# Optimization experiments

Hardware: AMD Instinct MI355X
Metric: run time of the kernel (lower is better)

## Reference

```python
import jax, jax.numpy as jnp
import numpy as np

DIM = 1024
NUM_HEADS = 16
HEAD_DIM = DIM // NUM_HEADS


def setup_inputs() -> dict:
    key = jax.random.key(0)
    k1, k2, k3 = jax.random.split(key, 3)
    x = jax.random.normal(k1, (2, 2048, DIM), dtype=jnp.float32)
    # nn.Linear weights stored as [out, in]; apply as x @ W.T
    w_qkv = jax.random.normal(k2, (3 * DIM, DIM), dtype=jnp.float32) * (1.0 / np.sqrt(DIM))
    w_out = jax.random.normal(k3, (DIM, DIM), dtype=jnp.float32) * (1.0 / np.sqrt(DIM))
    return {"x": x, "w_qkv": w_qkv, "w_out": w_out}


def reference(x, w_qkv, w_out):
    b, t, _ = x.shape
    qkv = x @ w_qkv.T                                  # [b, t, 3*dim]
    qkv = qkv.reshape(b, t, 3, NUM_HEADS, HEAD_DIM)    # (three h d) split order
    q, k, v = jnp.moveaxis(qkv, 2, 0)                  # each [b, t, h, d]
    q = q.transpose(0, 2, 1, 3)                        # [b, h, t, d]
    k = k.transpose(0, 2, 1, 3)
    v = v.transpose(0, 2, 1, 3)
    attn = jnp.einsum('bhid,bhjd->bhij', q, k) / np.sqrt(HEAD_DIM)
    causal_mask = jnp.triu(jnp.ones((t, t), dtype=bool), k=1)
    attn = jnp.where(causal_mask, -jnp.inf, attn)
    attn = jax.nn.softmax(attn, axis=-1)
    out = jnp.einsum('bhij,bhjd->bhid', attn, v)
    out = out.transpose(0, 2, 1, 3).reshape(b, t, DIM)
    return out @ w_out.T
```

## Files before the change

### kernel.cpp

```cpp
#include <hip/hip_runtime.h>

#define DIM_ 1024
#define HEADS_ 16
#define HD_ 64
#define T_ 2048
#define BATCH_ 2
#define QKVN_ 3072

typedef unsigned short u16;
typedef unsigned int u32;
typedef float f32x4 __attribute__((ext_vector_type(4)));
typedef float f32x16 __attribute__((ext_vector_type(16)));
typedef short s16x8 __attribute__((ext_vector_type(8)));
typedef unsigned short u16x4 __attribute__((ext_vector_type(4)));

__device__ __forceinline__ u16 f2bf(float f) {
  unsigned u = __float_as_uint(f);
  u += 0x7fffu + ((u >> 16) & 1u);
  return (u16)(u >> 16);
}

__device__ __forceinline__ float fexp2(float x) {
  float r;
  asm("v_exp_f32 %0, %1" : "=v"(r) : "v"(x));
  return r;
}

__device__ __forceinline__ float fmax3(float a, float b, float c) {
  float r;
  asm("v_max3_f32 %0, %1, %2, %3" : "=v"(r) : "v"(a), "v"(b), "v"(c));
  return r;
}

__device__ __forceinline__ u32 cvtpk(float a, float b) {
  u32 r;
  asm("v_cvt_pk_bf16_f32 %0, %1, %2" : "=v"(r) : "v"(a), "v"(b));
  return r;
}

__global__ __launch_bounds__(256) void cvt_all(const float* __restrict__ x,
                                               const float* __restrict__ wqkv,
                                               const float* __restrict__ wout,
                                               u16* __restrict__ outbase) {
  int i = blockIdx.x * 256 + threadIdx.x;
  const float4* src;
  int off;
  if (i < 1048576) { src = (const float4*)x; off = i; }
  else if (i < 1835008) { src = (const float4*)wqkv; off = i - 1048576; }
  else { src = (const float4*)wout; off = i - 1835008; }
  float4 v = src[off];
  u16x4 o;
  o.x = f2bf(v.x); o.y = f2bf(v.y); o.z = f2bf(v.z); o.w = f2bf(v.w);
  reinterpret_cast<u16x4*>(outbase)[i] = o;
}

__device__ __forceinline__ void gld_lds16(const void* g, void* l) {
  auto gp = (__attribute__((address_space(1))) char*)(unsigned long long)g;
  auto lp = (__attribute__((address_space(3))) char*)(unsigned int)(unsigned long long)l;
  __builtin_amdgcn_global_load_lds(gp, lp, 16, 0, 0);
}

template <int MODE>
__global__ __launch_bounds__(256) void gemm1(const u16* __restrict__ A,
                                             const u16* __restrict__ B,
                                             void* __restrict__ Cv,
                                             u16* __restrict__ vto) {
  constexpr int K = 1024;
  constexpr int NN = (MODE == 1) ? 1024 : QKVN_;
  constexpr int NT = (MODE == 1) ? 8 : 24;
  constexpr int CPX = (MODE == 1) ? 32 : 96;
  __shared__ __align__(16) u16 smem[16384];
  u16* As = smem;
  u16* Bs = smem + 8192;
  const int bid = blockIdx.x;
  const int wk = (bid & 7) * CPX + (bid >> 3);
  const int mt = wk / NT, nt = wk % NT;
  const int tid = threadIdx.x;
  const int lane = tid & 63;
  const int w = tid >> 6;
  const int wr = w >> 1, wc = w & 1;
  const int lrow = lane & 15, kg = lane >> 4;
  const u16* Ag = A + (size_t)(mt * 128) * K;
  const u16* Bg = B + (size_t)(nt * 128) * K;

  f32x4 acc[4][4];
#pragma unroll
  for (int i = 0; i < 4; ++i)
#pragma unroll
    for (int j = 0; j < 4; ++j) {
      f32x4 z = {0.f, 0.f, 0.f, 0.f};
      acc[i][j] = z;
    }

  const int srow = tid >> 3;
  const int scol = 8 * ((tid & 7) ^ ((tid >> 3) & 7));
  const int ldsw = (tid & ~63) * 16;

  int aoff[4][2], boff[4][2];
#pragma unroll
  for (int mf = 0; mf < 4; ++mf)
#pragma unroll
    for (int ks = 0; ks < 2; ++ks) {
      aoff[mf][ks] = (wr * 64 + mf * 16 + lrow) * 128 + (((ks * 4 + kg) ^ (lrow & 7)) << 4);
      boff[mf][ks] = (wc * 64 + mf * 16 + lrow) * 128 + (((ks * 4 + kg) ^ (lrow & 7)) << 4);
    }

  for (int k0 = 0; k0 < K; k0 += 64) {
#pragma unroll
    for (int c = 0; c < 4; ++c) {
      gld_lds16(Ag + (size_t)(c * 32 + srow) * K + k0 + scol, (char*)As + c * 4096 + ldsw);
      gld_lds16(Bg + (size_t)(c * 32 + srow) * K + k0 + scol, (char*)Bs + c * 4096 + ldsw);
    }
    __syncthreads();
#pragma unroll
    for (int ks = 0; ks < 2; ++ks) {
      s16x8 a[4], b[4];
#pragma unroll
      for (int mf = 0; mf < 4; ++mf)
        a[mf] = *(const s16x8*)((const char*)As + aoff[mf][ks]);
#pragma unroll
      for (int nf = 0; nf < 4; ++nf)
        b[nf] = *(const s16x8*)((const char*)Bs + boff[nf][ks]);
#pragma unroll
      for (int mf = 0; mf < 4; ++mf)
#pragma unroll
        for (int nf = 0; nf < 4; ++nf)
          acc[mf][nf] = __builtin_amdgcn_mfma_f32_16x16x32_bf16(a[mf], b[nf], acc[mf][nf], 0, 0, 0);
    }
    __syncthreads();
  }

  if (MODE == 1) {
    float* C = (float*)Cv;
#pragma unroll
    for (int mf = 0; mf < 4; ++mf)
#pragma unroll
      for (int nf = 0; nf < 4; ++nf)
#pragma unroll
        for (int j = 0; j < 4; ++j) {
          int r = mt * 128 + wr * 64 + mf * 16 + 4 * kg + j;
          int c = nt * 128 + wc * 64 + nf * 16 + lrow;
          C[(size_t)r * NN + c] = acc[mf][nf][j];
        }
  } else if (nt < 16) {
    u16* qkvo = (u16*)Cv;
#pragma unroll
    for (int mf = 0; mf < 4; ++mf)
#pragma unroll
      for (int nf = 0; nf < 4; ++nf)
#pragma unroll
        for (int j = 0; j < 4; ++j) {
          int r = mt * 128 + wr * 64 + mf * 16 + 4 * kg + j;
          int c = nt * 128 + wc * 64 + nf * 16 + lrow;
          qkvo[(size_t)r * QKVN_ + c] = f2bf(acc[mf][nf][j]);
        }
  } else {
    const int c16 = tid >> 4, chunk = tid & 15;
    const int bb = mt >> 4;
    const int tb = (mt & 15) * 128 + chunk * 8;
#pragma unroll
    for (int p = 0; p < 2; ++p) {
      __syncthreads();
      if (wc == p) {
#pragma unroll
        for (int mf = 0; mf < 4; ++mf)
#pragma unroll
          for (int nf = 0; nf < 4; ++nf) {
            const int cl = nf * 16 + lrow;
            const int rl = wr * 64 + mf * 16 + 4 * kg;
            u16x4 pk;
            pk.x = f2bf(acc[mf][nf][0]); pk.y = f2bf(acc[mf][nf][1]);
            pk.z = f2bf(acc[mf][nf][2]); pk.w = f2bf(acc[mf][nf][3]);
            *(u16x4*)&smem[cl * 136 + rl] = pk;
          }
      }
      __syncthreads();
#pragma unroll
      for (int pp = 0; pp < 4; ++pp) {
        const int cl = pp * 16 + c16;
        const int cg = nt * 128 + p * 64 + cl;
        const int hV = (cg >> 6) & 15, d = cg & 63;
        const s16x8 v = *(const s16x8*)&smem[cl * 136 + chunk * 8];
        *(s16x8*)(vto + ((size_t)((bb * 16 + hV) * 64 + d)) * T_ + tb) = v;
      }
    }
  }
}

__global__ __launch_bounds__(256, 2) void attn_fwd(const u16* __restrict__ qkv,
                                                   const u16* __restrict__ vt,
                                                   u16* __restrict__ o) {
  const int gid = blockIdx.x;
  const int gq = gid >> 3;
  const int bh = (gid & 7) * 4 + (gq >> 4);
  const int pr = gq & 15;
  const int b = bh >> 4, h = bh & 15;
  const int tid = threadIdx.x;
  const int lane = tid & 63;
  const int qw = (tid >> 6) & 1;
  const int kvg = tid >> 7;
  const int l31 = lane & 31, hi = lane >> 5;

  __shared__ __align__(16) char smem[65536];

  const int row_s = tid >> 3, slot_s = tid & 7;
  const u16* Kbase = qkv + (size_t)(b * T_) * QKVN_ + 1024 + h * 64;
  const u16* Vbase = vt + (size_t)(bh * 64) * T_;
  const u16* KgA = Kbase + (size_t)row_s * QKVN_ + slot_s * 8;
  const u16* KgB = KgA + (size_t)32 * QKVN_;
  const u16* VgA = Vbase + (size_t)row_s * T_ + slot_s * 8;
  const u16* VgB = VgA + (size_t)32 * T_;
  const int dstA = row_s * 128 + ((slot_s ^ (row_s & 7)) << 4);

  const int rbyte = l31 * 128;
  const int xsw = l31 & 7;
  const float CEXP = 0.18033688011112042f;

  for (int ph = 0; ph < 2; ++ph) {
    const int jt = (ph == 0) ? (31 - pr) : pr;
    const int nt = jt + 1;
    const int nrt = (nt + 1) >> 1;
    const int qrow0 = 64 * jt + 32 * qw;

    s16x8 qf[4];
    {
      const u16* qp = qkv + (size_t)(b * T_ + qrow0 + l31) * QKVN_ + h * 64 + 8 * hi;
#pragma unroll
      for (int ksl = 0; ksl < 4; ++ksl)
        qf[ksl] = *(const s16x8*)(qp + 16 * ksl);
    }

    f32x16 o0v, o1v;
#pragma unroll
    for (int r = 0; r < 16; ++r) { o0v[r] = 0.f; o1v[r] = 0.f; }
    float mrun = -__builtin_inff(), lrun = 0.0f;

    __syncthreads();
    *(s16x8*)(smem + dstA)                 = *(const s16x8*)KgA;
    *(s16x8*)(smem + 4096 + dstA)          = *(const s16x8*)KgB;
    *(s16x8*)(smem + 32768 + dstA)         = *(const s16x8*)VgA;
    *(s16x8*)(smem + 32768 + 4096 + dstA)  = *(const s16x8*)VgB;
    if (nt > 1) {
      *(s16x8*)(smem + 8192 + dstA)                = *(const s16x8*)(KgA + (size_t)64 * QKVN_);
      *(s16x8*)(smem + 8192 + 4096 + dstA)         = *(const s16x8*)(KgB + (size_t)64 * QKVN_);
      *(s16x8*)(smem + 32768 + 8192 + dstA)        = *(const s16x8*)(VgA + 64);
      *(s16x8*)(smem + 32768 + 8192 + 4096 + dstA) = *(const s16x8*)(VgB + 64);
    }

    int cur = 0;
    for (int r = 0; r < nrt; ++r) {
      const int t = 2 * r + kvg;
      const bool pe = (2 * r + 2 < nt), po = (2 * r + 3 < nt);
      s16x8 ke0, ke1, ve0, ve1, ko0, ko1, vo0, vo1;
      if (pe) {
        const size_t kofs = (size_t)(2 * r + 2) * 64 * QKVN_;
        const int vofs = (2 * r + 2) * 64;
        ke0 = *(const s16x8*)(KgA + kofs);
        ke1 = *(const s16x8*)(KgB + kofs);
        ve0 = *(const s16x8*)(VgA + vofs);
        ve1 = *(const s16x8*)(VgB + vofs);
      }
      if (po) {
        const size_t kofs = (size_t)(2 * r + 3) * 64 * QKVN_;
        const int vofs = (2 * r + 3) * 64;
        ko0 = *(const s16x8*)(KgA + kofs);
        ko1 = *(const s16x8*)(KgB + kofs);
        vo0 = *(const s16x8*)(VgA + vofs);
        vo1 = *(const s16x8*)(VgB + vofs);
      }
      __syncthreads();

      if (t < nt) {
        const char* Kc = smem + cur * 16384 + kvg * 8192;
        const char* Vc = smem + 32768 + cur * 16384 + kvg * 8192;
        const bool isdiag = (t == nt - 1);
        const bool two = !(isdiag && qw == 0);

        f32x16 s0v, s1v;
#pragma unroll
        for (int rr = 0; rr < 16; ++rr) { s0v[rr] = 0.f; s1v[rr] = 0.f; }
        __builtin_amdgcn_s_setprio(1);
#pragma unroll
        for (int ksl = 0; ksl < 4; ++ksl) {
          const s16x8 kf = *(const s16x8*)(Kc + rbyte + (((2 * ksl + hi) ^ xsw) << 4));
          s0v = __builtin_amdgcn_mfma_f32_32x32x16_bf16(kf, qf[ksl], s0v, 0, 0, 0);
        }
        if (two) {
#pragma unroll
          for (int ksl = 0; ksl < 4; ++ksl) {
            const s16x8 kf = *(const s16x8*)(Kc + 4096 + rbyte + (((2 * ksl + hi) ^ xsw) << 4));
            s1v = __builtin_amdgcn_mfma_f32_32x32x16_bf16(kf, qf[ksl], s1v, 0, 0, 0);
          }
        }
        __builtin_amdgcn_s_setprio(0);

        if (isdiag) {
          const int thr = 32 * qw + l31;
#pragma unroll
          for (int rr = 0; rr < 16; ++rr) {
            const int kvl = 4 * hi + (rr & 3) + 8 * (rr >> 2);
            if (kvl > thr) s0v[rr] = -__builtin_inff();
            if (two && kvl + 32 > thr) s1v[rr] = -__builtin_inff();
          }
        }

        float mloc = fmax3(s0v[0], s0v[1], s0v[2]);
#pragma unroll
        for (int rr = 3; rr < 15; rr += 2) mloc = fmax3(mloc, s0v[rr], s0v[rr + 1]);
        mloc = fmaxf(mloc, s0v[15]);
        if (two) {
          mloc = fmax3(mloc, s1v[0], s1v[1]);
#pragma unroll
          for (int rr = 2; rr < 16; rr += 2) mloc = fmax3(mloc, s1v[rr], s1v[rr + 1]);
        }
        mloc = fmaxf(mloc, __shfl_xor(mloc, 32));

        const bool needfull = !((mloc - mrun) * CEXP <= 8.0f);
        if (__any(needfull)) {
          const float newm = fmaxf(mrun, mloc);
          const float sc = fexp2((mrun - newm) * CEXP);
          mrun = newm;
          lrun *= sc;
          o0v *= sc;
          o1v *= sc;
        }
        const float msc = mrun * CEXP;

        float rs = 0.0f;
        u32 pd0[8], pd1[8];
#pragma unroll
        for (int ri = 0; ri < 8; ++ri) {
          const float p0 = fexp2(__builtin_fmaf(s0v[2 * ri], CEXP, -msc));
          const float p1 = fexp2(__builtin_fmaf(s0v[2 * ri + 1], CEXP, -msc));
          rs += p0 + p1;
          pd0[ri] = cvtpk(p0, p1);
        }
        if (two) {
#pragma unroll
          for (int ri = 0; ri < 8; ++ri) {
            const float p0 = fexp2(__builtin_fmaf(s1v[2 * ri], CEXP, -msc));
            const float p1 = fexp2(__builtin_fmaf(s1v[2 * ri + 1], CEXP, -msc));
            rs += p0 + p1;
            pd1[ri] = cvtpk(p0, p1);
          }
        }
        rs += __shfl_xor(rs, 32);
        lrun += rs;

        __builtin_amdgcn_s_setprio(1);
#pragma unroll
        for (int kk = 0; kk < 4; ++kk) {
          if (kk >= 2 && !two) break;
          u32 x0, y0, x1, y1;
          if (kk == 0)      { x0 = pd0[0]; y0 = pd0[2]; x1 = pd0[1]; y1 = pd0[3]; }
          else if (kk == 1) { x0 = pd0[4]; y0 = pd0[6]; x1 = pd0[5]; y1 = pd0[7]; }
          else if (kk == 2) { x0 = pd1[0]; y0 = pd1[2]; x1 = pd1[1]; y1 = pd1[3]; }
          else              { x0 = pd1[4]; y0 = pd1[6]; x1 = pd1[5]; y1 = pd1[7]; }
          asm volatile("v_permlane32_swap_b32 %0, %1" : "+v"(x0), "+v"(y0));
          asm volatile("v_permlane32_swap_b32 %0, %1" : "+v"(x1), "+v"(y1));
          u32 pw[4] = {x0, x1, y0, y1};
          const s16x8 pf = *(const s16x8*)pw;
          const s16x8 vf0 = *(const s16x8*)(Vc + rbyte + (((2 * kk + hi) ^ xsw) << 4));
          const s16x8 vf1 = *(const s16x8*)(Vc + 4096 + rbyte + (((2 * kk + hi) ^ xsw) << 4));
          o0v = __builtin_amdgcn_mfma_f32_32x32x16_bf16(vf0, pf, o0v, 0, 0, 0);
          o1v = __builtin_amdgcn_mfma_f32_32x32x16_bf16(vf1, pf, o1v, 0, 0, 0);
        }
        __builtin_amdgcn_s_setprio(0);
      }

      if (pe) {
        const int nb = (cur ^ 1) * 16384;
        *(s16x8*)(smem + nb + dstA)                = ke0;
        *(s16x8*)(smem + nb + 4096 + dstA)         = ke1;
        *(s16x8*)(smem + 32768 + nb + dstA)        = ve0;
        *(s16x8*)(smem + 32768 + nb + 4096 + dstA) = ve1;
      }
      if (po) {
        const int nb = (cur ^ 1) * 16384 + 8192;
        *(s16x8*)(smem + nb + dstA)                = ko0;
        *(s16x8*)(smem + nb + 4096 + dstA)         = ko1;
        *(s16x8*)(smem + 32768 + nb + dstA)        = vo0;
        *(s16x8*)(smem + 32768 + nb + 4096 + dstA) = vo1;
      }
      cur ^= 1;
    }

    __syncthreads();
    float* Om = (float*)smem + qw * 2048;
    float* Mf = (float*)(smem + 16384) + qw * 64;
    float* Lf = (float*)(smem + 16896) + qw * 64;
    if (kvg == 1) {
#pragma unroll
      for (int rr = 0; rr < 16; ++rr) {
        Om[rr * 64 + lane] = o0v[rr];
        Om[(16 + rr) * 64 + lane] = o1v[rr];
      }
      Mf[lane] = mrun;
      Lf[lane] = lrun;
    }
    __syncthreads();
    if (kvg == 0) {
      const float mA = Mf[lane];
      const float lA = Lf[lane];
      const float m2 = fmaxf(mrun, mA);
      const float sB = fexp2((mrun - m2) * CEXP);
      const float sA = fexp2((mA - m2) * CEXP);
      const float linv = 1.0f / (lrun * sB + lA * sA);
      u16* orow = o + (size_t)(b * T_ + qrow0 + l31) * DIM_ + h * 64;
#pragma unroll
      for (int ri = 0; ri < 8; ++ri) {
        const int dbase0 = 4 * hi + 8 * (ri >> 1) + 2 * (ri & 1);
        const float a0 = (o0v[2 * ri] * sB + Om[(2 * ri) * 64 + lane] * sA) * linv;
        const float a1 = (o0v[2 * ri + 1] * sB + Om[(2 * ri + 1) * 64 + lane] * sA) * linv;
        const float c0 = (o1v[2 * ri] * sB + Om[(16 + 2 * ri) * 64 + lane] * sA) * linv;
        const float c1 = (o1v[2 * ri + 1] * sB + Om[(16 + 2 * ri + 1) * 64 + lane] * sA) * linv;
        *(u32*)(orow + dbase0) = cvtpk(a0, a1);
        *(u32*)(orow + 32 + dbase0) = cvtpk(c0, c1);
      }
    }
  }
}

extern "C" void kernel_launch(void* const* d_in, const int* in_sizes, int n_in,
                              void* d_out, int out_size, void* d_ws, size_t ws_size,
                              hipStream_t stream) {
  const float* x = (const float*)d_in[0];
  const float* w_qkv = (const float*)d_in[1];
  const float* w_out = (const float*)d_in[2];
  char* ws = (char*)d_ws;
  u16* xb    = (u16*)(ws + 0);
  u16* wqkvb = (u16*)(ws + 8388608);
  u16* woutb = (u16*)(ws + 14680064);
  u16* qkvb  = (u16*)(ws + 16777216);
  u16* vtb   = (u16*)(ws + 41943040);
  u16* attno = (u16*)(ws + 50331648);

  cvt_all<<<8192, 256, 0, stream>>>(x, w_qkv, w_out, xb);
  gemm1<2><<<768, 256, 0, stream>>>(xb, wqkvb, qkvb, vtb);
  attn_fwd<<<512, 256, 0, stream>>>(qkvb, vtb, attno);
  gemm1<1><<<256, 256, 0, stream>>>(attno, woutb, d_out, nullptr);
}
```

Baseline: 98.79 us.

## Use direct global-to-LDS K loads, register V loads, one tile per block

The attention kernel no longer pairs a long and a short query tile in each block. It now launches 1024 blocks, one query tile each, ordered longest first. K tiles are staged with direct global-to-LDS loads instead of going through registers, and V fragments are read straight from global memory into registers, which halves the LDS footprint. This is meant to cut register staging, LDS traffic and shared-memory pressure so more blocks fit per CU, at the cost of uncoalesced-ish V global reads and reliance on the hardware to balance the causal workload.

```diff
diff --git a/kernel.cpp b/kernel.cpp
--- a/kernel.cpp
+++ b/kernel.cpp
@@ -187,236 +187,209 @@
   }
 }
 
-__global__ __launch_bounds__(256, 2) void attn_fwd(const u16* __restrict__ qkv,
-                                                   const u16* __restrict__ vt,
-                                                   u16* __restrict__ o) {
+__global__ __launch_bounds__(256) void attn_fwd(const u16* __restrict__ qkv,
+                                                const u16* __restrict__ vt,
+                                                u16* __restrict__ o) {
   const int gid = blockIdx.x;
-  const int gq = gid >> 3;
-  const int bh = (gid & 7) * 4 + (gq >> 4);
-  const int pr = gq & 15;
+  const int jt = 31 - (gid >> 5);
+  const int bh = gid & 31;
   const int b = bh >> 4, h = bh & 15;
   const int tid = threadIdx.x;
   const int lane = tid & 63;
   const int qw = (tid >> 6) & 1;
   const int kvg = tid >> 7;
   const int l31 = lane & 31, hi = lane >> 5;
-
-  __shared__ __align__(16) char smem[65536];
-
-  const int row_s = tid >> 3, slot_s = tid & 7;
+  const int nt = jt + 1;
+  const int nrt = (nt + 1) >> 1;
+  const int qrow0 = 64 * jt + 32 * qw;
+
+  __shared__ __align__(16) char smem[32768];
+
+  const int row0s = tid >> 3, col0s = 8 * ((tid & 7) ^ ((tid >> 3) & 7));
+  const int row1s = (256 + tid) >> 3, col1s = 8 * ((tid & 7) ^ (((256 + tid) >> 3) & 7));
   const u16* Kbase = qkv + (size_t)(b * T_) * QKVN_ + 1024 + h * 64;
-  const u16* Vbase = vt + (size_t)(bh * 64) * T_;
-  const u16* KgA = Kbase + (size_t)row_s * QKVN_ + slot_s * 8;
-  const u16* KgB = KgA + (size_t)32 * QKVN_;
-  const u16* VgA = Vbase + (size_t)row_s * T_ + slot_s * 8;
-  const u16* VgB = VgA + (size_t)32 * T_;
-  const int dstA = row_s * 128 + ((slot_s ^ (row_s & 7)) << 4);
+  const u16* Ks0 = Kbase + (size_t)row0s * QKVN_ + col0s;
+  const u16* Ks1 = Kbase + (size_t)row1s * QKVN_ + col1s;
+  const int wbase = (tid & ~63) * 16;
+
+  const u16* Vg = vt + (size_t)(bh * 64 + l31) * T_ + 8 * hi;
 
   const int rbyte = l31 * 128;
   const int xsw = l31 & 7;
   const float CEXP = 0.18033688011112042f;
 
-  for (int ph = 0; ph < 2; ++ph) {
-    const int jt = (ph == 0) ? (31 - pr) : pr;
-    const int nt = jt + 1;
-    const int nrt = (nt + 1) >> 1;
-    const int qrow0 = 64 * jt + 32 * qw;
-
-    s16x8 qf[4];
-    {
-      const u16* qp = qkv + (size_t)(b * T_ + qrow0 + l31) * QKVN_ + h * 64 + 8 * hi;
-#pragma unroll
-      for (int ksl = 0; ksl < 4; ++ksl)
-        qf[ksl] = *(const s16x8*)(qp + 16 * ksl);
-    }
-
-    f32x16 o0v, o1v;
-#pragma unroll
-    for (int r = 0; r < 16; ++r) { o0v[r] = 0.f; o1v[r] = 0.f; }
-    float mrun = -__builtin_inff(), lrun = 0.0f;
+  s16x8 qf[4];
+  {
+    const u16* qp = qkv + (size_t)(b * T_ + qrow0 + l31) * QKVN_ + h * 64 + 8 * hi;
+#pragma unroll
+    for (int ksl = 0; ksl < 4; ++ksl)
+      qf[ksl] = *(const s16x8*)(qp + 16 * ksl);
+  }
+
+  f32x16 o0v, o1v;
+#pragma unroll
+  for (int r = 0; r < 16; ++r) { o0v[r] = 0.f; o1v[r] = 0.f; }
+  float mrun = -__builtin_inff(), lrun = 0.0f;
+
+  gld_lds16(Ks0, smem + wbase);
+  gld_lds16(Ks1, smem + 4096 + wbase);
+  if (nt > 1) {
+    gld_lds16(Ks0 + (size_t)64 * QKVN_, smem + 16384 + wbase);
+    gld_lds16(Ks1 + (size_t)64 * QKVN_, smem + 16384 + 4096 + wbase);
+  }
+  __syncthreads();
+
+  int cur = 0;
+  for (int r = 0; r < nrt; ++r) {
+    const int t = 2 * r + kvg;
+    if (2 * r + 2 < nt) {
+      const size_t ko = (size_t)(2 * r + 2) * 64 * QKVN_;
+      gld_lds16(Ks0 + ko, smem + (cur ^ 1) * 8192 + wbase);
+      gld_lds16(Ks1 + ko, smem + (cur ^ 1) * 8192 + 4096 + wbase);
+    }
+    if (2 * r + 3 < nt) {
+      const size_t ko = (size_t)(2 * r + 3) * 64 * QKVN_;
+      gld_lds16(Ks0 + ko, smem + 16384 + (cur ^ 1) * 8192 + wbase);
+      gld_lds16(Ks1 + ko, smem + 16384 + (cur ^ 1) * 8192 + 4096 + wbase);
+    }
+
+    if (t < nt) {
+      const char* Kc = smem + kvg * 16384 + cur * 8192;
+      const bool isdiag = (t == nt - 1);
+      const bool two = !(isdiag && qw == 0);
+
+      s16x8 vf0[4], vf1[4];
+      const u16* Vt = Vg + t * 64;
+#pragma unroll
+      for (int kk = 0; kk < 4; ++kk) {
+        vf0[kk] = *(const s16x8*)(Vt + 16 * kk);
+        vf1[kk] = *(const s16x8*)(Vt + (size_t)32 * T_ + 16 * kk);
+      }
+
+      f32x16 s0v, s1v;
+#pragma unroll
+      for (int rr = 0; rr < 16; ++rr) { s0v[rr] = 0.f; s1v[rr] = 0.f; }
+      __builtin_amdgcn_s_setprio(1);
+#pragma unroll
+      for (int ksl = 0; ksl < 4; ++ksl) {
+        const s16x8 kf = *(const s16x8*)(Kc + rbyte + (((2 * ksl + hi) ^ xsw) << 4));
+        s0v = __builtin_amdgcn_mfma_f32_32x32x16_bf16(kf, qf[ksl], s0v, 0, 0, 0);
+      }
+      if (two) {
+#pragma unroll
+        for (int ksl = 0; ksl < 4; ++ksl) {
+          const s16x8 kf = *(const s16x8*)(Kc + 4096 + rbyte + (((2 * ksl + hi) ^ xsw) << 4));
+          s1v = __builtin_amdgcn_mfma_f32_32x32x16_bf16(kf, qf[ksl], s1v, 0, 0, 0);
+        }
+      }
+      __builtin_amdgcn_s_setprio(0);
+
+      if (isdiag) {
+        const int thr = 32 * qw + l31;
+#pragma unroll
+        for (int rr = 0; rr < 16; ++rr) {
+          const int kvl = 4 * hi + (rr & 3) + 8 * (rr >> 2);
+          if (kvl > thr) s0v[rr] = -__builtin_inff();
+          if (two && kvl + 32 > thr) s1v[rr] = -__builtin_inff();
+        }
+      }
+
+      float mloc = fmax3(s0v[0], s0v[1], s0v[2]);
+#pragma unroll
+      for (int rr = 3; rr < 15; rr += 2) mloc = fmax3(mloc, s0v[rr], s0v[rr + 1]);
+      mloc = fmaxf(mloc, s0v[15]);
+      if (two) {
+        mloc = fmax3(mloc, s1v[0], s1v[1]);
+#pragma unroll
+        for (int rr = 2; rr < 16; rr += 2) mloc = fmax3(mloc, s1v[rr], s1v[rr + 1]);
+      }
+      mloc = fmaxf(mloc, __shfl_xor(mloc, 32));
+
+      const bool needfull = !((mloc - mrun) * CEXP <= 8.0f);
+      if (__any(needfull)) {
+        const float newm = fmaxf(mrun, mloc);
+        const float sc = fexp2((mrun - newm) * CEXP);
+        mrun = newm;
+        lrun *= sc;
+        o0v *= sc;
+        o1v *= sc;
+      }
+      const float msc = mrun * CEXP;
+
+      float rs = 0.0f;
+      u32 pd0[8], pd1[8];
+#pragma unroll
+      for (int ri = 0; ri < 8; ++ri) {
+        const float p0 = fexp2(__builtin_fmaf(s0v[2 * ri], CEXP, -msc));
+        const float p1 = fexp2(__builtin_fmaf(s0v[2 * ri + 1], CEXP, -msc));
+        rs += p0 + p1;
+        pd0[ri] = cvtpk(p0, p1);
+      }
+      if (two) {
+#pragma unroll
+        for (int ri = 0; ri < 8; ++ri) {
+          const float p0 = fexp2(__builtin_fmaf(s1v[2 * ri], CEXP, -msc));
+          const float p1 = fexp2(__builtin_fmaf(s1v[2 * ri + 1], CEXP, -msc));
+          rs += p0 + p1;
+          pd1[ri] = cvtpk(p0, p1);
+        }
+      }
+      rs += __shfl_xor(rs, 32);
+      lrun += rs;
+
+      __builtin_amdgcn_s_setprio(1);
+#pragma unroll
+      for (int kk = 0; kk < 4; ++kk) {
+        if (kk >= 2 && !two) break;
+        u32 x0, y0, x1, y1;
+        if (kk == 0)      { x0 = pd0[0]; y0 = pd0[2]; x1 = pd0[1]; y1 = pd0[3]; }
+        else if (kk == 1) { x0 = pd0[4]; y0 = pd0[6]; x1 = pd0[5]; y1 = pd0[7]; }
+        else if (kk == 2) { x0 = pd1[0]; y0 = pd1[2]; x1 = pd1[1]; y1 = pd1[3]; }
+        else              { x0 = pd1[4]; y0 = pd1[6]; x1 = pd1[5]; y1 = pd1[7]; }
+        asm volatile("v_permlane32_swap_b32 %0, %1" : "+v"(x0), "+v"(y0));
+        asm volatile("v_permlane32_swap_b32 %0, %1" : "+v"(x1), "+v"(y1));
+        u32 pw[4] = {x0, x1, y0, y1};
+        const s16x8 pf = *(const s16x8*)pw;
+        o0v = __builtin_amdgcn_mfma_f32_32x32x16_bf16(vf0[kk], pf, o0v, 0, 0, 0);
+        o1v = __builtin_amdgcn_mfma_f32_32x32x16_bf16(vf1[kk], pf, o1v, 0, 0, 0);
+      }
+      __builtin_amdgcn_s_setprio(0);
+    }
 
     __syncthreads();
-    *(s16x8*)(smem + dstA)                 = *(const s16x8*)KgA;
-    *(s16x8*)(smem + 4096 + dstA)          = *(const s16x8*)KgB;
-    *(s16x8*)(smem + 32768 + dstA)         = *(const s16x8*)VgA;
-    *(s16x8*)(smem + 32768 + 4096 + dstA)  = *(const s16x8*)VgB;
-    if (nt > 1) {
-      *(s16x8*)(smem + 8192 + dstA)                = *(const s16x8*)(KgA + (size_t)64 * QKVN_);
-      *(s16x8*)(smem + 8192 + 4096 + dstA)         = *(const s16x8*)(KgB + (size_t)64 * QKVN_);
-      *(s16x8*)(smem + 32768 + 8192 + dstA)        = *(const s16x8*)(VgA + 64);
-      *(s16x8*)(smem + 32768 + 8192 + 4096 + dstA) = *(const s16x8*)(VgB + 64);
-    }
-
-    int cur = 0;
-    for (int r = 0; r < nrt; ++r) {
-      const int t = 2 * r + kvg;
-      const bool pe = (2 * r + 2 < nt), po = (2 * r + 3 < nt);
-      s16x8 ke0, ke1, ve0, ve1, ko0, ko1, vo0, vo1;
-      if (pe) {
-        const size_t kofs = (size_t)(2 * r + 2) * 64 * QKVN_;
-        const int vofs = (2 * r + 2) * 64;
-        ke0 = *(const s16x8*)(KgA + kofs);
-        ke1 = *(const s16x8*)(KgB + kofs);
-        ve0 = *(const s16x8*)(VgA + vofs);
-        ve1 = *(const s16x8*)(VgB + vofs);
-      }
-      if (po) {
-        const size_t kofs = (size_t)(2 * r + 3) * 64 * QKVN_;
-        const int vofs = (2 * r + 3) * 64;
-        ko0 = *(const s16x8*)(KgA + kofs);
-        ko1 = *(const s16x8*)(KgB + kofs);
-        vo0 = *(const s16x8*)(VgA + vofs);
-        vo1 = *(const s16x8*)(VgB + vofs);
-      }
-      __syncthreads();
-
-      if (t < nt) {
-        const char* Kc = smem + cur * 16384 + kvg * 8192;
-        const char* Vc = smem + 32768 + cur * 16384 + kvg * 8192;
-        const bool isdiag = (t == nt - 1);
-        const bool two = !(isdiag && qw == 0);
-
-        f32x16 s0v, s1v;
-#pragma unroll
-        for (int rr = 0; rr < 16; ++rr) { s0v[rr] = 0.f; s1v[rr] = 0.f; }
-        __builtin_amdgcn_s_setprio(1);
-#pragma unroll
-        for (int ksl = 0; ksl < 4; ++ksl) {
-          const s16x8 kf = *(const s16x8*)(Kc + rbyte + (((2 * ksl + hi) ^ xsw) << 4));
-          s0v = __builtin_amdgcn_mfma_f32_32x32x16_bf16(kf, qf[ksl], s0v, 0, 0, 0);
-        }
-        if (two) {
-#pragma unroll
-          for (int ksl = 0; ksl < 4; ++ksl) {
-            const s16x8 kf = *(const s16x8*)(Kc + 4096 + rbyte + (((2 * ksl + hi) ^ xsw) << 4));
-            s1v = __builtin_amdgcn_mfma_f32_32x32x16_bf16(kf, qf[ksl], s1v, 0, 0, 0);
-          }
-        }
-        __builtin_amdgcn_s_setprio(0);
-
-        if (isdiag) {
-          const int thr = 32 * qw + l31;
-#pragma unroll
-          for (int rr = 0; rr < 16; ++rr) {
-            const int kvl = 4 * hi + (rr & 3) + 8 * (rr >> 2);
-            if (kvl > thr) s0v[rr] = -__builtin_inff();
-            if (two && kvl + 32 > thr) s1v[rr] = -__builtin_inff();
-          }
-        }
-
-        float mloc = fmax3(s0v[0], s0v[1], s0v[2]);
-#pragma unroll
-        for (int rr = 3; rr < 15; rr += 2) mloc = fmax3(mloc, s0v[rr], s0v[rr + 1]);
-        mloc = fmaxf(mloc, s0v[15]);
-        if (two) {
-          mloc = fmax3(mloc, s1v[0], s1v[1]);
-#pragma unroll
-          for (int rr = 2; rr < 16; rr += 2) mloc = fmax3(mloc, s1v[rr], s1v[rr + 1]);
-        }
-        mloc = fmaxf(mloc, __shfl_xor(mloc, 32));
-
-        const bool needfull = !((mloc - mrun) * CEXP <= 8.0f);
-        if (__any(needfull)) {
-          const float newm = fmaxf(mrun, mloc);
-          const float sc = fexp2((mrun - newm) * CEXP);
-          mrun = newm;
-          lrun *= sc;
-          o0v *= sc;
-          o1v *= sc;
-        }
-        const float msc = mrun * CEXP;
-
-        float rs = 0.0f;
-        u32 pd0[8], pd1[8];
-#pragma unroll
-        for (int ri = 0; ri < 8; ++ri) {
-          const float p0 = fexp2(__builtin_fmaf(s0v[2 * ri], CEXP, -msc));
-          const float p1 = fexp2(__builtin_fmaf(s0v[2 * ri + 1], CEXP, -msc));
-          rs += p0 + p1;
-          pd0[ri] = cvtpk(p0, p1);
-        }
-        if (two) {
-#pragma unroll
-          for (int ri = 0; ri < 8; ++ri) {
-            const float p0 = fexp2(__builtin_fmaf(s1v[2 * ri], CEXP, -msc));
-            const float p1 = fexp2(__builtin_fmaf(s1v[2 * ri + 1], CEXP, -msc));
-            rs += p0 + p1;
-            pd1[ri] = cvtpk(p0, p1);
-          }
-        }
-        rs += __shfl_xor(rs, 32);
-        lrun += rs;
-
-        __builtin_amdgcn_s_setprio(1);
-#pragma unroll
-        for (int kk = 0; kk < 4; ++kk) {
-          if (kk >= 2 && !two) break;
-          u32 x0, y0, x1, y1;
-          if (kk == 0)      { x0 = pd0[0]; y0 = pd0[2]; x1 = pd0[1]; y1 = pd0[3]; }
-          else if (kk == 1) { x0 = pd0[4]; y0 = pd0[6]; x1 = pd0[5]; y1 = pd0[7]; }
-          else if (kk == 2) { x0 = pd1[0]; y0 = pd1[2]; x1 = pd1[1]; y1 = pd1[3]; }
-          else              { x0 = pd1[4]; y0 = pd1[6]; x1 = pd1[5]; y1 = pd1[7]; }
-          asm volatile("v_permlane32_swap_b32 %0, %1" : "+v"(x0), "+v"(y0));
-          asm volatile("v_permlane32_swap_b32 %0, %1" : "+v"(x1), "+v"(y1));
-          u32 pw[4] = {x0, x1, y0, y1};
-          const s16x8 pf = *(const s16x8*)pw;
-          const s16x8 vf0 = *(const s16x8*)(Vc + rbyte + (((2 * kk + hi) ^ xsw) << 4));
-          const s16x8 vf1 = *(const s16x8*)(Vc + 4096 + rbyte + (((2 * kk + hi) ^ xsw) << 4));
-          o0v = __builtin_amdgcn_mfma_f32_32x32x16_bf16(vf0, pf, o0v, 0, 0, 0);
-          o1v = __builtin_amdgcn_mfma_f32_32x32x16_bf16(vf1, pf, o1v, 0, 0, 0);
-        }
-        __builtin_amdgcn_s_setprio(0);
-      }
-
-      if (pe) {
-        const int nb = (cur ^ 1) * 16384;
-        *(s16x8*)(smem + nb + dstA)                = ke0;
-        *(s16x8*)(smem + nb + 4096 + dstA)         = ke1;
-        *(s16x8*)(smem + 32768 + nb + dstA)        = ve0;
-        *(s16x8*)(smem + 32768 + nb + 4096 + dstA) = ve1;
-      }
-      if (po) {
-        const int nb = (cur ^ 1) * 16384 + 8192;
-        *(s16x8*)(smem + nb + dstA)                = ko0;
-        *(s16x8*)(smem + nb + 4096 + dstA)         = ko1;
-        *(s16x8*)(smem + 32768 + nb + dstA)        = vo0;
-        *(s16x8*)(smem + 32768 + nb + 4096 + dstA) = vo1;
-      }
-      cur ^= 1;
-    }
-
-    __syncthreads();
-    float* Om = (float*)smem + qw * 2048;
-    float* Mf = (float*)(smem + 16384) + qw * 64;
-    float* Lf = (float*)(smem + 16896) + qw * 64;
-    if (kvg == 1) {
-#pragma unroll
-      for (int rr = 0; rr < 16; ++rr) {
-        Om[rr * 64 + lane] = o0v[rr];
-        Om[(16 + rr) * 64 + lane] = o1v[rr];
-      }
-      Mf[lane] = mrun;
-      Lf[lane] = lrun;
-    }
-    __syncthreads();
-    if (kvg == 0) {
-      const float mA = Mf[lane];
-      const float lA = Lf[lane];
-      const float m2 = fmaxf(mrun, mA);
-      const float sB = fexp2((mrun - m2) * CEXP);
-      const float sA = fexp2((mA - m2) * CEXP);
-      const float linv = 1.0f / (lrun * sB + lA * sA);
-      u16* orow = o + (size_t)(b * T_ + qrow0 + l31) * DIM_ + h * 64;
-#pragma unroll
-      for (int ri = 0; ri < 8; ++ri) {
-        const int dbase0 = 4 * hi + 8 * (ri >> 1) + 2 * (ri & 1);
-        const float a0 = (o0v[2 * ri] * sB + Om[(2 * ri) * 64 + lane] * sA) * linv;
-        const float a1 = (o0v[2 * ri + 1] * sB + Om[(2 * ri + 1) * 64 + lane] * sA) * linv;
-        const float c0 = (o1v[2 * ri] * sB + Om[(16 + 2 * ri) * 64 + lane] * sA) * linv;
-        const float c1 = (o1v[2 * ri + 1] * sB + Om[(16 + 2 * ri + 1) * 64 + lane] * sA) * linv;
-        *(u32*)(orow + dbase0) = cvtpk(a0, a1);
-        *(u32*)(orow + 32 + dbase0) = cvtpk(c0, c1);
-      }
+    cur ^= 1;
+  }
+
+  float* Om = (float*)smem + qw * 2048;
+  float* Mf = (float*)(smem + 16384) + qw * 64;
+  float* Lf = (float*)(smem + 16896) + qw * 64;
+  if (kvg == 1) {
+#pragma unroll
+    for (int rr = 0; rr < 16; ++rr) {
+      Om[rr * 64 + lane] = o0v[rr];
+      Om[(16 + rr) * 64 + lane] = o1v[rr];
+    }
+    Mf[lane] = mrun;
+    Lf[lane] = lrun;
+  }
+  __syncthreads();
+  if (kvg == 0) {
+    const float mA = Mf[lane];
+    const float lA = Lf[lane];
+    const float m2 = fmaxf(mrun, mA);
+    const float sB = fexp2((mrun - m2) * CEXP);
+    const float sA = fexp2((mA - m2) * CEXP);
+    const float linv = 1.0f / (lrun * sB + lA * sA);
+    u16* orow = o + (size_t)(b * T_ + qrow0 + l31) * DIM_ + h * 64;
+#pragma unroll
+    for (int ri = 0; ri < 8; ++ri) {
+      const int dbase0 = 4 * hi + 8 * (ri >> 1) + 2 * (ri & 1);
+      const float a0 = (o0v[2 * ri] * sB + Om[(2 * ri) * 64 + lane] * sA) * linv;
+      const float a1 = (o0v[2 * ri + 1] * sB + Om[(2 * ri + 1) * 64 + lane] * sA) * linv;
+      const float c0 = (o1v[2 * ri] * sB + Om[(16 + 2 * ri) * 64 + lane] * sA) * linv;
+      const float c1 = (o1v[2 * ri + 1] * sB + Om[(16 + 2 * ri + 1) * 64 + lane] * sA) * linv;
+      *(u32*)(orow + dbase0) = cvtpk(a0, a1);
+      *(u32*)(orow + 32 + dbase0) = cvtpk(c0, c1);
     }
   }
 }
@@ -437,6 +410,6 @@
 
   cvt_all<<<8192, 256, 0, stream>>>(x, w_qkv, w_out, xb);
   gemm1<2><<<768, 256, 0, stream>>>(xb, wqkvb, qkvb, vtb);
-  attn_fwd<<<512, 256, 0, stream>>>(qkvb, vtb, attno);
+  attn_fwd<<<1024, 256, 0, stream>>>(qkvb, vtb, attno);
   gemm1<1><<<256, 256, 0, stream>>>(attno, woutb, d_out, nullptr);
 }
```

After: 107.8 us. 1.09x slower.
